# Kernel tuning notes

Hardware: AMD Instinct MI355X
Metric: run time of the kernel (lower is better)

Reference implementation:

```python
import jax, jax.numpy as jnp
import numpy as np

T, B, F = 512, 256, 1
H = 256          # hidden width of all GRU stacks
P = 256          # pred_classes
DELAY = 1
W_SCALE = 0.06   # ~1/sqrt(H), mimics torch GRUCell init scale


def setup_inputs() -> dict:
    key = jax.random.key(0)
    ks = jax.random.split(key, 24)
    rn = lambda k, shp, s=1.0: s * jax.random.normal(k, shp, dtype=jnp.float32)
    return {
        "sequence": rn(ks[0], (T, B, F)),
        "delay_pad": rn(ks[1], (DELAY, B, F)),
        "h0_enc": rn(ks[2], (B, H)),
        "h0_mask": rn(ks[3], (B, H)),
        "h0_pred": rn(ks[4], (B, H)),
        "enc_w_ih": rn(ks[5], (3 * H, F), W_SCALE),
        "enc_w_hh": rn(ks[6], (3 * H, H), W_SCALE),
        "enc_b_ih": rn(ks[7], (3 * H,), W_SCALE),
        "enc_b_hh": rn(ks[8], (3 * H,), W_SCALE),
        "mdec_w_ih": rn(ks[9], (3 * H, H), W_SCALE),
        "mdec_w_hh": rn(ks[10], (3 * H, H), W_SCALE),
        "mdec_b_ih": rn(ks[11], (3 * H,), W_SCALE),
        "mdec_b_hh": rn(ks[12], (3 * H,), W_SCALE),
        "mlin_w": rn(ks[13], (F, H), W_SCALE),
        "mlin_b": rn(ks[14], (F,), W_SCALE),
        "pdec_w_ih": rn(ks[15], (3 * H, H), W_SCALE),
        "pdec_w_hh": rn(ks[16], (3 * H, H), W_SCALE),
        "pdec_b_ih": rn(ks[17], (3 * H,), W_SCALE),
        "pdec_b_hh": rn(ks[18], (3 * H,), W_SCALE),
        "plin_w": rn(ks[19], (P, H), W_SCALE),
        "plin_b": rn(ks[20], (P,), W_SCALE),
    }


def gru_cell(x, h, w_ih, w_hh, b_ih, b_hh):
    # torch.nn.GRUCell semantics; gate order r, z, n in the stacked weights.
    gi = x @ w_ih.T + b_ih           # [B, 3H]
    gh = h @ w_hh.T + b_hh           # [B, 3H]
    i_r, i_z, i_n = jnp.split(gi, 3, axis=-1)
    h_r, h_z, h_n = jnp.split(gh, 3, axis=-1)
    r = jax.nn.sigmoid(i_r + h_r)
    z = jax.nn.sigmoid(i_z + h_z)
    n = jnp.tanh(i_n + r * h_n)
    return (1.0 - z) * n + z * h


def reference(sequence, delay_pad, h0_enc, h0_mask, h0_pred,
              enc_w_ih, enc_w_hh, enc_b_ih, enc_b_hh,
              mdec_w_ih, mdec_w_hh, mdec_b_ih, mdec_b_hh, mlin_w, mlin_b,
              pdec_w_ih, pdec_w_hh, pdec_b_ih, pdec_b_hh, plin_w, plin_b):
    # delay: prepend padding, drop last `delay` steps.  seq stays [T, B, F].
    seq = jnp.concatenate([delay_pad, sequence[:-DELAY]], axis=0)

    def step(carry, x_t):
        h_e, h_m, h_p = carry
        h_e = gru_cell(x_t, h_e, enc_w_ih, enc_w_hh, enc_b_ih, enc_b_hh)
        h_m = gru_cell(h_e, h_m, mdec_w_ih, mdec_w_hh, mdec_b_ih, mdec_b_hh)
        mask_t = h_m @ mlin_w.T + mlin_b      # [B, F]
        h_p = gru_cell(h_e, h_p, pdec_w_ih, pdec_w_hh, pdec_b_ih, pdec_b_hh)
        pred_t = h_p @ plin_w.T + plin_b      # [B, P]
        return (h_e, h_m, h_p), (mask_t, pred_t)

    _, (masks, preds) = jax.lax.scan(step, (h0_enc, h0_mask, h0_pred), seq)
    mask = masks.reshape(seq.shape)           # [T, B, F]
    pred = jnp.mean(preds, axis=0)            # [B, P]
    return mask, pred
```

## Files before the change

kernel.cpp:

```cpp
#include <hip/hip_runtime.h>
#include <hip/hip_fp16.h>

typedef _Float16 f16;
typedef _Float16 f16x8 __attribute__((ext_vector_type(8)));
typedef _Float16 f16x4 __attribute__((ext_vector_type(4)));
typedef float    f32x4 __attribute__((ext_vector_type(4)));

#define TT 512
#define BB 256
#define HH 256

#define O_WFRAG_ENC 0u
#define O_WFRAG_M   393216u
#define O_WFRAG_P   786432u
#define O_WFRAG_GI  1179648u
#define O_HE_ST     1966080u
#define O_HM_ST     2097152u
#define O_HP_ST     2228224u
#define O_HPSUM     2359296u
#define O_DYN       2621440u
#define DYN_PER_STEP 917504u

__device__ __forceinline__ float sigf(float x){ return 1.0f/(1.0f+__expf(-x)); }
__device__ __forceinline__ float tanh_(float x){
  float xc = fminf(fmaxf(x,-15.f),15.f);
  float e  = __expf(2.f*xc);
  return (e-1.f)/(e+1.f);
}
__device__ __forceinline__ int hswz(int row, int j){
  return row*256 + ((((j>>3) ^ (row&7)))<<3) + (j&7);
}
__device__ __forceinline__ void gload_lds16(const void* g, void* l){
  __builtin_amdgcn_global_load_lds(
      (const __attribute__((address_space(1))) unsigned int*)g,
      (__attribute__((address_space(3))) unsigned int*)l, 16, 0, 0);
}

__global__ void prep_kernel(
    const float* __restrict__ enc_whh, const float* __restrict__ mdec_whh,
    const float* __restrict__ pdec_whh, const float* __restrict__ mdec_wih,
    const float* __restrict__ pdec_wih,
    const float* __restrict__ h0e, const float* __restrict__ h0m, const float* __restrict__ h0p,
    f16* __restrict__ wfrag_enc, f16* __restrict__ wfrag_m, f16* __restrict__ wfrag_p,
    f16* __restrict__ wfrag_gi,
    f16* __restrict__ he_st, f16* __restrict__ hm_st, f16* __restrict__ hp_st,
    float* __restrict__ hpsum)
{
  int idx = blockIdx.x*256 + threadIdx.x;
  const int NW = 16*3*8*64*8;
  if (idx < 3*NW){
    int b = idx / NW, e = idx % NW;
    int jj = e & 7, l = (e>>3)&63, ks = (e>>9)&7, t2 = e>>12;
    int g = t2 % 3, w = t2 / 3;
    int row = g*256 + w*16 + (l&15);
    int col = ks*32 + (l>>4)*8 + jj;
    const float* W = (b==0)?enc_whh:((b==1)?mdec_whh:pdec_whh);
    f16* D = (b==0)?wfrag_enc:((b==1)?wfrag_m:wfrag_p);
    D[e] = (f16)W[row*256+col];
    return;
  }
  idx -= 3*NW;
  const int NG = 96*8*64*8;
  if (idx < NG){
    int e = idx;
    int jj = e&7, l=(e>>3)&63, ks=(e>>9)&7, mt = e>>12;
    int row = mt*16 + (l&15);
    int col = ks*32 + (l>>4)*8 + jj;
    float v = (row < 768) ? mdec_wih[row*256+col] : pdec_wih[(row-768)*256+col];
    wfrag_gi[e] = (f16)v;
    return;
  }
  idx -= NG;
  if (idx < 65536){
    he_st[idx] = (f16)h0e[idx];
    hm_st[idx] = (f16)h0m[idx];
    hp_st[idx] = (f16)h0p[idx];
    hpsum[idx] = 0.f;
  }
}

template<int MODE>
__device__ __forceinline__ void gru_run(
  int bt, int slice, int SL,
  const f16* __restrict__ wfrag,
  const float* __restrict__ bih, const float* __restrict__ bhh,
  const float* __restrict__ enc_wih,
  const float* __restrict__ seq, const float* __restrict__ dpad,
  const f16* __restrict__ gi_src,
  f16* __restrict__ h_state,
  f16* __restrict__ he_buf,
  const float* __restrict__ mlin_w, const float* __restrict__ mlin_b,
  float* __restrict__ out_mask,
  float* __restrict__ hpsum,
  unsigned char* smem)
{
  const int tid = threadIdx.x;
  const int lane = tid & 63;
  const int wid  = tid >> 6;
  const int l15  = lane & 15;
  const int lhi  = lane >> 4;
  const int bi0  = lhi*4;
  const int b0   = bt*16;

  f16* hbuf  = (f16*)smem;
  f16* gib   = (f16*)(smem + 16384);
  float* xb  = (float*)(smem + 16384 + 49152);
  float* mred = xb + 32;

  f16x8 wf[2][3][8];
  #pragma unroll
  for (int q=0;q<2;++q){
    const int w = wid*2+q;
    #pragma unroll
    for (int g=0;g<3;++g)
      #pragma unroll
      for (int ks=0;ks<8;++ks)
        wf[q][g][ks] = *(const f16x8*)(wfrag + ((size_t)(((w*3+g)*8)+ks)*64 + lane)*8);
  }
  #pragma unroll
  for (int q=0;q<2;++q)
    #pragma unroll
    for (int g=0;g<3;++g)
      #pragma unroll
      for (int ks=0;ks<8;++ks)
        asm volatile("" : "+v"(wf[q][g][ks]));

  float cr[2], cz[2], cnh[2], cni[2];
  float wr_[2], wz_[2], wn_[2], mw[2];
  #pragma unroll
  for (int q=0;q<2;++q){
    const int j = (wid*2+q)*16 + l15;
    cr[q]  = bih[j]     + bhh[j];
    cz[q]  = bih[256+j] + bhh[256+j];
    cnh[q] = bhh[512+j];
    cni[q] = bih[512+j];
    if (MODE==0){ wr_[q]=enc_wih[j]; wz_[q]=enc_wih[256+j]; wn_[q]=enc_wih[512+j]; }
    if (MODE==1){ mw[q]=mlin_w[j]; }
  }
  #pragma unroll
  for (int q=0;q<2;++q){
    const int j = (wid*2+q)*16 + l15;
    #pragma unroll
    for (int r=0;r<4;++r)
      hbuf[hswz(bi0+r, j)] = h_state[(size_t)(b0+bi0+r)*256 + j];
  }
  if (MODE==0){
    if (tid<16){
      const int t = slice*SL;
      xb[tid] = (t==0) ? dpad[b0+tid] : seq[(size_t)(t-1)*BB + b0 + tid];
    }
  } else {
    #pragma unroll
    for (int k=0;k<3;++k){
      const int c = wid*3 + k;
      gload_lds16((const char*)gi_src + c*1024 + (lane<<4),
                  (char*)gib + c*1024);
    }
  }
  __syncthreads();

  float psum[2][4];
  if (MODE==2){
    #pragma unroll
    for (int q=0;q<2;++q)
      #pragma unroll
      for (int r=0;r<4;++r) psum[q][r]=0.f;
  }

  for (int ts=0; ts<SL; ++ts){
    const int cur = ts & 1;
    f16* hc = hbuf + cur*4096;
    f16* hn = hbuf + (cur^1)*4096;

    if (MODE==0){
      if (tid<16 && ts+1<SL){
        const int t = slice*SL + ts + 1;
        xb[(cur^1)*16 + tid] = seq[(size_t)(t-1)*BB + b0 + tid];
      }
    } else {
      if (ts+1 < SL){
        const char* gsrc = (const char*)gi_src + (size_t)(ts+1)*786432u;
        char* gdst = (char*)gib + (cur^1)*24576;
        #pragma unroll
        for (int k=0;k<3;++k){
          const int c = wid*3 + k;
          gload_lds16(gsrc + c*1024 + (lane<<4), gdst + c*1024);
        }
      }
    }
    if (MODE==1){
      if (tid<16 && ts>0){
        float v = mlin_b[0];
        #pragma unroll
        for (int w=0;w<8;++w) v += mred[(cur^1)*128 + w*16 + tid];
        out_mask[(size_t)(slice*SL + ts-1)*BB + b0 + tid] = v;
      }
    }

    float mpart[4] = {0.f,0.f,0.f,0.f};
    #pragma unroll
    for (int q=0;q<2;++q){
      const int j = (wid*2+q)*16 + l15;
      f32x4 a0 = {cr[q],cr[q],cr[q],cr[q]};
      f32x4 a1 = {cz[q],cz[q],cz[q],cz[q]};
      f32x4 a2 = {cnh[q],cnh[q],cnh[q],cnh[q]};
      #pragma unroll
      for (int ks=0;ks<8;++ks){
        const f16x8 a = *(const f16x8*)(hc + l15*256 + ((((ks*4+lhi) ^ (l15&7)))<<3));
        a0 = __builtin_amdgcn_mfma_f32_16x16x32_f16(a, wf[q][0][ks], a0, 0,0,0);
        a1 = __builtin_amdgcn_mfma_f32_16x16x32_f16(a, wf[q][1][ks], a1, 0,0,0);
        a2 = __builtin_amdgcn_mfma_f32_16x16x32_f16(a, wf[q][2][ks], a2, 0,0,0);
      }
      float gir[4], giz[4], gin[4];
      if (MODE==0){
        #pragma unroll
        for (int r=0;r<4;++r){
          const float x = xb[cur*16 + bi0 + r];
          gir[r]=x*wr_[q]; giz[r]=x*wz_[q]; gin[r]=x*wn_[q];
        }
      } else {
        const f16* gb = gib + cur*12288;
        const f16x4 g0v = *(const f16x4*)(gb + j*16 + bi0);
        const f16x4 g1v = *(const f16x4*)(gb + (256+j)*16 + bi0);
        const f16x4 g2v = *(const f16x4*)(gb + (512+j)*16 + bi0);
        #pragma unroll
        for (int r=0;r<4;++r){ gir[r]=(float)g0v[r]; giz[r]=(float)g1v[r]; gin[r]=(float)g2v[r]; }
      }
      #pragma unroll
      for (int r=0;r<4;++r){
        const int sz = hswz(bi0+r, j);
        const float hprev = (float)hc[sz];
        const float rr = sigf(gir[r] + a0[r]);
        const float zz = sigf(giz[r] + a1[r]);
        const float nn = tanh_(gin[r] + cni[q] + rr*a2[r]);
        const float h  = (1.f-zz)*nn + zz*hprev;
        hn[sz] = (f16)h;
        if (MODE==0) he_buf[((size_t)ts*BB + (b0+bi0+r))*HH + j] = (f16)h;
        if (MODE==1) mpart[r] += h*mw[q];
        if (MODE==2) psum[q][r] += h;
      }
    }
    if (MODE==1){
      #pragma unroll
      for (int m=1;m<16;m<<=1){
        #pragma unroll
        for (int r=0;r<4;++r) mpart[r] += __shfl_xor(mpart[r], m, 64);
      }
      if (l15==0){
        #pragma unroll
        for (int r=0;r<4;++r) mred[cur*128 + wid*16 + bi0 + r] = mpart[r];
      }
    }
    __syncthreads();
  }

  if (MODE==1 && tid<16){
    float v = mlin_b[0];
    #pragma unroll
    for (int w=0;w<8;++w) v += mred[((SL-1)&1)*128 + w*16 + tid];
    out_mask[(size_t)(slice*SL + SL-1)*BB + b0 + tid] = v;
  }
  {
    const f16* hf = hbuf + (SL&1)*4096;
    #pragma unroll
    for (int q=0;q<2;++q){
      const int j = (wid*2+q)*16 + l15;
      #pragma unroll
      for (int r=0;r<4;++r)
        h_state[(size_t)(b0+bi0+r)*256 + j] = hf[hswz(bi0+r, j)];
    }
  }
  if (MODE==2){
    #pragma unroll
    for (int q=0;q<2;++q){
      const int j = (wid*2+q)*16 + l15;
      #pragma unroll
      for (int r=0;r<4;++r){
        const size_t idx = (size_t)(b0+bi0+r)*256 + j;
        hpsum[idx] = hpsum[idx] + psum[q][r];
      }
    }
  }
}

__global__ __launch_bounds__(512,1) void rec_kernel(
  const float* __restrict__ seq, const float* __restrict__ dpad,
  const float* __restrict__ enc_wih, const float* __restrict__ enc_bih, const float* __restrict__ enc_bhh,
  const float* __restrict__ mdec_bih, const float* __restrict__ mdec_bhh,
  const float* __restrict__ pdec_bih, const float* __restrict__ pdec_bhh,
  const float* __restrict__ mlin_w, const float* __restrict__ mlin_b,
  const f16* __restrict__ wfrag_enc, const f16* __restrict__ wfrag_m, const f16* __restrict__ wfrag_p,
  f16* __restrict__ he_st, f16* __restrict__ hm_st, f16* __restrict__ hp_st,
  f16* __restrict__ he_buf, const f16* __restrict__ gi_buf,
  float* __restrict__ hpsum, float* __restrict__ out_mask,
  int dec_slice, int enc_slice, int n_dec, int SL)
{
  __shared__ __align__(16) unsigned char smem[16384 + 49152 + 128 + 1024];
  const int bid = blockIdx.x;
  if (bid < n_dec){
    const int rec = bid >> 4, bt = bid & 15;
    const f16* gsrc = gi_buf + ((size_t)bt*1536 + (size_t)rec*768)*16;
    if (rec==0)
      gru_run<1>(bt, dec_slice, SL, wfrag_m, mdec_bih, mdec_bhh, nullptr, nullptr, nullptr,
                 gsrc, hm_st, nullptr, mlin_w, mlin_b, out_mask, nullptr, smem);
    else
      gru_run<2>(bt, dec_slice, SL, wfrag_p, pdec_bih, pdec_bhh, nullptr, nullptr, nullptr,
                 gsrc, hp_st, nullptr, nullptr, nullptr, nullptr, hpsum, smem);
  } else {
    const int bt = bid - n_dec;
    gru_run<0>(bt, enc_slice, SL, wfrag_enc, enc_bih, enc_bhh, enc_wih, seq, dpad,
               nullptr, he_st, he_buf, nullptr, nullptr, nullptr, nullptr, smem);
  }
}

__global__ __launch_bounds__(256,4) void gi_kernel(
  const f16* __restrict__ he_buf, const f16* __restrict__ wfrag_gi,
  f16* __restrict__ gi_buf)
{
  const int ts = blockIdx.x >> 2;
  const int bq = blockIdx.x & 3;
  const int tid = threadIdx.x, lane = tid&63, wid = tid>>6;
  const int l15 = lane&15, lhi = lane>>4;
  __shared__ f16 het[64*264];
  {
    const uint4* src = (const uint4*)(he_buf + ((size_t)ts*BB + bq*64)*HH);
    uint4* dst = (uint4*)het;
    #pragma unroll
    for (int k=0;k<8;++k){
      const int i = tid + k*256;
      dst[(i>>5)*33 + (i&31)] = src[i];
    }
  }
  __syncthreads();
  for (int mi=0; mi<24; ++mi){
    const int mt = wid*24 + mi;
    f32x4 acc[4] = {{0,0,0,0},{0,0,0,0},{0,0,0,0},{0,0,0,0}};
    #pragma unroll
    for (int ks=0;ks<8;++ks){
      const f16x8 a = *(const f16x8*)(wfrag_gi + ((size_t)(mt*8+ks)*64 + lane)*8);
      #pragma unroll
      for (int bt=0;bt<4;++bt){
        const f16x8 b = *(const f16x8*)(het + (bt*16+l15)*264 + ks*32 + lhi*8);
        acc[bt] = __builtin_amdgcn_mfma_f32_16x16x32_f16(a, b, acc[bt], 0,0,0);
      }
    }
    #pragma unroll
    for (int bt=0;bt<4;++bt){
      const int btg = bq*4 + bt;
      const size_t base = (((size_t)ts*16 + btg)*1536 + (size_t)mt*16 + lhi*4)*16 + l15;
      #pragma unroll
      for (int r=0;r<4;++r) gi_buf[base + (size_t)r*16] = (f16)acc[bt][r];
    }
  }
}

__global__ __launch_bounds__(256,1) void pred_kernel(
  const float* __restrict__ hpsum, const float* __restrict__ plin_w,
  const float* __restrict__ plin_b, float* __restrict__ out)
{
  __shared__ float hs[256];
  const int p = threadIdx.x;
  const float bias = plin_b[p];
  for (int bb=0; bb<4; ++bb){
    const int b = blockIdx.x*4 + bb;
    __syncthreads();
    hs[p] = hpsum[(size_t)b*256 + p];
    __syncthreads();
    float acc = 0.f;
    const float4* wrow = (const float4*)(plin_w + (size_t)p*256);
    #pragma unroll 4
    for (int k4=0;k4<64;++k4){
      const float4 w = wrow[k4];
      acc += hs[k4*4+0]*w.x + hs[k4*4+1]*w.y + hs[k4*4+2]*w.z + hs[k4*4+3]*w.w;
    }
    out[131072 + (size_t)b*256 + p] = acc*(1.f/512.f) + bias;
  }
}

extern "C" void kernel_launch(void* const* d_in, const int* in_sizes, int n_in,
                              void* d_out, int out_size, void* d_ws, size_t ws_size,
                              hipStream_t stream)
{
  const float* seq      = (const float*)d_in[0];
  const float* dpad     = (const float*)d_in[1];
  const float* h0e      = (const float*)d_in[2];
  const float* h0m      = (const float*)d_in[3];
  const float* h0p      = (const float*)d_in[4];
  const float* enc_wih  = (const float*)d_in[5];
  const float* enc_whh  = (const float*)d_in[6];
  const float* enc_bih  = (const float*)d_in[7];
  const float* enc_bhh  = (const float*)d_in[8];
  const float* mdec_wih = (const float*)d_in[9];
  const float* mdec_whh = (const float*)d_in[10];
  const float* mdec_bih = (const float*)d_in[11];
  const float* mdec_bhh = (const float*)d_in[12];
  const float* mlin_w   = (const float*)d_in[13];
  const float* mlin_b   = (const float*)d_in[14];
  const float* pdec_wih = (const float*)d_in[15];
  const float* pdec_whh = (const float*)d_in[16];
  const float* pdec_bih = (const float*)d_in[17];
  const float* pdec_bhh = (const float*)d_in[18];
  const float* plin_w   = (const float*)d_in[19];
  const float* plin_b   = (const float*)d_in[20];
  float* out = (float*)d_out;

  char* ws = (char*)d_ws;
  f16* wfrag_enc = (f16*)(ws + O_WFRAG_ENC);
  f16* wfrag_m   = (f16*)(ws + O_WFRAG_M);
  f16* wfrag_p   = (f16*)(ws + O_WFRAG_P);
  f16* wfrag_gi  = (f16*)(ws + O_WFRAG_GI);
  f16* he_st     = (f16*)(ws + O_HE_ST);
  f16* hm_st     = (f16*)(ws + O_HM_ST);
  f16* hp_st     = (f16*)(ws + O_HP_ST);
  float* hpsum   = (float*)(ws + O_HPSUM);

  int SL = 64;
  while (SL > 1 && (size_t)O_DYN + (size_t)SL*DYN_PER_STEP > ws_size) SL >>= 1;
  const int S = TT / SL;
  f16* he_buf = (f16*)(ws + O_DYN);
  f16* gi_buf = (f16*)(ws + O_DYN + (size_t)SL*131072u);

  prep_kernel<<<dim3(4096), dim3(256), 0, stream>>>(
      enc_whh, mdec_whh, pdec_whh, mdec_wih, pdec_wih, h0e, h0m, h0p,
      wfrag_enc, wfrag_m, wfrag_p, wfrag_gi, he_st, hm_st, hp_st, hpsum);

  rec_kernel<<<dim3(16), dim3(512), 0, stream>>>(
      seq, dpad, enc_wih, enc_bih, enc_bhh, mdec_bih, mdec_bhh, pdec_bih, pdec_bhh,
      mlin_w, mlin_b, wfrag_enc, wfrag_m, wfrag_p, he_st, hm_st, hp_st,
      he_buf, gi_buf, hpsum, out, 0, 0, 0, SL);
  gi_kernel<<<dim3(SL*4), dim3(256), 0, stream>>>(he_buf, wfrag_gi, gi_buf);

  for (int s=0; s<S; ++s){
    const int has_enc = (s+1 < S);
    rec_kernel<<<dim3(has_enc?48:32), dim3(512), 0, stream>>>(
        seq, dpad, enc_wih, enc_bih, enc_bhh, mdec_bih, mdec_bhh, pdec_bih, pdec_bhh,
        mlin_w, mlin_b, wfrag_enc, wfrag_m, wfrag_p, he_st, hm_st, hp_st,
        he_buf, gi_buf, hpsum, out, s, s+1, 32, SL);
    if (has_enc)
      gi_kernel<<<dim3(SL*4), dim3(256), 0, stream>>>(he_buf, wfrag_gi, gi_buf);
  }

  pred_kernel<<<dim3(64), dim3(256), 0, stream>>>(hpsum, plin_w, plin_b, out);
}
```

Before: 3.423 ms.

## Split each GRU recurrence across two cooperating blocks with flag-based hidden-state exchange

Each recurrent batch tile is now handled by a pair of 256-thread blocks, each owning half of the hidden units. After every timestep the two blocks exchange their halves of the new hidden state through global memory, using release/acquire flags and a spin-wait. This doubles the CUs working on the serial recurrence and halves the weight registers each block holds, at the cost of a per-step cross-block handshake. The change also folds the input biases into gi_kernel, reads gi values directly from global instead of staging them through LDS, and computes the mask projection with a separate in-block reduction; it relies on all 96 blocks being co-resident to avoid deadlock.

```diff
diff --git a/kernel.cpp b/kernel.cpp
--- a/kernel.cpp
+++ b/kernel.cpp
@@ -5,6 +5,8 @@
 typedef _Float16 f16x8 __attribute__((ext_vector_type(8)));
 typedef _Float16 f16x4 __attribute__((ext_vector_type(4)));
 typedef float    f32x4 __attribute__((ext_vector_type(4)));
+typedef unsigned long long u64;
+typedef u64 u64x2 __attribute__((ext_vector_type(2)));
 
 #define TT 512
 #define BB 256
@@ -18,7 +20,9 @@
 #define O_HM_ST     2097152u
 #define O_HP_ST     2228224u
 #define O_HPSUM     2359296u
-#define O_DYN       2621440u
+#define O_XCHG      2621440u
+#define O_FLAGS     3407872u
+#define O_DYN       3408896u
 #define DYN_PER_STEP 917504u
 
 __device__ __forceinline__ float sigf(float x){ return 1.0f/(1.0f+__expf(-x)); }
@@ -29,11 +33,6 @@
 }
 __device__ __forceinline__ int hswz(int row, int j){
   return row*256 + ((((j>>3) ^ (row&7)))<<3) + (j&7);
-}
-__device__ __forceinline__ void gload_lds16(const void* g, void* l){
-  __builtin_amdgcn_global_load_lds(
-      (const __attribute__((address_space(1))) unsigned int*)g,
-      (__attribute__((address_space(3))) unsigned int*)l, 16, 0, 0);
 }
 
 __global__ void prep_kernel(
@@ -44,7 +43,7 @@
     f16* __restrict__ wfrag_enc, f16* __restrict__ wfrag_m, f16* __restrict__ wfrag_p,
     f16* __restrict__ wfrag_gi,
     f16* __restrict__ he_st, f16* __restrict__ hm_st, f16* __restrict__ hp_st,
-    float* __restrict__ hpsum)
+    float* __restrict__ hpsum, int* __restrict__ flags)
 {
   int idx = blockIdx.x*256 + threadIdx.x;
   const int NW = 16*3*8*64*8;
@@ -76,12 +75,13 @@
     hm_st[idx] = (f16)h0m[idx];
     hp_st[idx] = (f16)h0p[idx];
     hpsum[idx] = 0.f;
+    if (idx < 96) flags[idx] = 0;
   }
 }
 
 template<int MODE>
 __device__ __forceinline__ void gru_run(
-  int bt, int slice, int SL,
+  int role, int bt, int slice, int SL,
   const f16* __restrict__ wfrag,
   const float* __restrict__ bih, const float* __restrict__ bhh,
   const float* __restrict__ enc_wih,
@@ -92,6 +92,7 @@
   const float* __restrict__ mlin_w, const float* __restrict__ mlin_b,
   float* __restrict__ out_mask,
   float* __restrict__ hpsum,
+  u64* __restrict__ xchg, int* __restrict__ flags,
   unsigned char* smem)
 {
   const int tid = threadIdx.x;
@@ -101,16 +102,16 @@
   const int lhi  = lane >> 4;
   const int bi0  = lhi*4;
   const int b0   = bt*16;
-
-  f16* hbuf  = (f16*)smem;
-  f16* gib   = (f16*)(smem + 16384);
-  float* xb  = (float*)(smem + 16384 + 49152);
-  float* mred = xb + 32;
+  constexpr int FREC = (MODE==1) ? 0 : ((MODE==2) ? 1 : 2);
+
+  f16* hbuf   = (f16*)smem;
+  float* xb   = (float*)(smem + 16384);
+  float* mlwf = xb + 32;
 
   f16x8 wf[2][3][8];
   #pragma unroll
   for (int q=0;q<2;++q){
-    const int w = wid*2+q;
+    const int w = role*8 + wid*2 + q;
     #pragma unroll
     for (int g=0;g<3;++g)
       #pragma unroll
@@ -126,20 +127,30 @@
         asm volatile("" : "+v"(wf[q][g][ks]));
 
   float cr[2], cz[2], cnh[2], cni[2];
-  float wr_[2], wz_[2], wn_[2], mw[2];
+  float wr_[2], wz_[2], wn_[2];
   #pragma unroll
   for (int q=0;q<2;++q){
-    const int j = (wid*2+q)*16 + l15;
-    cr[q]  = bih[j]     + bhh[j];
-    cz[q]  = bih[256+j] + bhh[256+j];
-    cnh[q] = bhh[512+j];
-    cni[q] = bih[512+j];
-    if (MODE==0){ wr_[q]=enc_wih[j]; wz_[q]=enc_wih[256+j]; wn_[q]=enc_wih[512+j]; }
-    if (MODE==1){ mw[q]=mlin_w[j]; }
-  }
-  #pragma unroll
-  for (int q=0;q<2;++q){
-    const int j = (wid*2+q)*16 + l15;
+    const int j = (role*8 + wid*2 + q)*16 + l15;
+    if (MODE==0){
+      cr[q]  = bih[j]     + bhh[j];
+      cz[q]  = bih[256+j] + bhh[256+j];
+      cnh[q] = bhh[512+j];
+      cni[q] = bih[512+j];
+      wr_[q]=enc_wih[j]; wz_[q]=enc_wih[256+j]; wn_[q]=enc_wih[512+j];
+    } else {
+      cr[q]  = bhh[j];
+      cz[q]  = bhh[256+j];
+      cnh[q] = bhh[512+j];
+    }
+  }
+  float mlb = 0.f;
+  if (MODE==1 && role==0){
+    mlwf[tid] = mlin_w[tid];
+    mlb = mlin_b[0];
+  }
+
+  for (int jb=wid; jb<16; jb+=4){
+    const int j = jb*16 + l15;
     #pragma unroll
     for (int r=0;r<4;++r)
       hbuf[hswz(bi0+r, j)] = h_state[(size_t)(b0+bi0+r)*256 + j];
@@ -149,13 +160,6 @@
       const int t = slice*SL;
       xb[tid] = (t==0) ? dpad[b0+tid] : seq[(size_t)(t-1)*BB + b0 + tid];
     }
-  } else {
-    #pragma unroll
-    for (int k=0;k<3;++k){
-      const int c = wid*3 + k;
-      gload_lds16((const char*)gi_src + c*1024 + (lane<<4),
-                  (char*)gib + c*1024);
-    }
   }
   __syncthreads();
 
@@ -166,41 +170,44 @@
       #pragma unroll
       for (int r=0;r<4;++r) psum[q][r]=0.f;
   }
+
+  const int fmy = (FREC*16 + bt)*2 + role;
+  const int fpt = (FREC*16 + bt)*2 + (1-role);
+  int* myf = flags + fmy;
+  int* ptf = flags + fpt;
 
   for (int ts=0; ts<SL; ++ts){
     const int cur = ts & 1;
     f16* hc = hbuf + cur*4096;
     f16* hn = hbuf + (cur^1)*4096;
-
-    if (MODE==0){
-      if (tid<16 && ts+1<SL){
-        const int t = slice*SL + ts + 1;
-        xb[(cur^1)*16 + tid] = seq[(size_t)(t-1)*BB + b0 + tid];
-      }
+    const int gstep = slice*SL + ts;
+
+    f16x4 gv[2][3];
+    if (MODE!=0){
+      const f16* gts = gi_src + (size_t)ts*393216u;
+      #pragma unroll
+      for (int q=0;q<2;++q)
+        #pragma unroll
+        for (int g=0;g<3;++g)
+          gv[q][g] = *(const f16x4*)(gts + ((size_t)(g*256 + (role*8+wid*2+q)*16 + l15))*16 + bi0);
     } else {
-      if (ts+1 < SL){
-        const char* gsrc = (const char*)gi_src + (size_t)(ts+1)*786432u;
-        char* gdst = (char*)gib + (cur^1)*24576;
-        #pragma unroll
-        for (int k=0;k<3;++k){
-          const int c = wid*3 + k;
-          gload_lds16(gsrc + c*1024 + (lane<<4), gdst + c*1024);
-        }
-      }
-    }
-    if (MODE==1){
-      if (tid<16 && ts>0){
-        float v = mlin_b[0];
-        #pragma unroll
-        for (int w=0;w<8;++w) v += mred[(cur^1)*128 + w*16 + tid];
-        out_mask[(size_t)(slice*SL + ts-1)*BB + b0 + tid] = v;
-      }
-    }
-
-    float mpart[4] = {0.f,0.f,0.f,0.f};
+      if (tid<16 && ts+1<SL)
+        xb[(cur^1)*16 + tid] = seq[(size_t)(slice*SL + ts)*BB + b0 + tid];
+    }
+
+    if (MODE==1 && role==0 && ts>0){
+      const int mb = tid>>4, jj = tid&15;
+      float s = 0.f;
+      #pragma unroll
+      for (int k=0;k<16;++k){ const int j = jj + k*16; s += (float)hc[hswz(mb, j)]*mlwf[j]; }
+      s += __shfl_xor(s,1,64); s += __shfl_xor(s,2,64);
+      s += __shfl_xor(s,4,64); s += __shfl_xor(s,8,64);
+      if (jj==0) out_mask[(size_t)(slice*SL + ts-1)*BB + b0 + mb] = s + mlb;
+    }
+
     #pragma unroll
     for (int q=0;q<2;++q){
-      const int j = (wid*2+q)*16 + l15;
+      const int j = (role*8 + wid*2 + q)*16 + l15;
       f32x4 a0 = {cr[q],cr[q],cr[q],cr[q]};
       f32x4 a1 = {cz[q],cz[q],cz[q],cz[q]};
       f32x4 a2 = {cnh[q],cnh[q],cnh[q],cnh[q]};
@@ -216,15 +223,13 @@
         #pragma unroll
         for (int r=0;r<4;++r){
           const float x = xb[cur*16 + bi0 + r];
-          gir[r]=x*wr_[q]; giz[r]=x*wz_[q]; gin[r]=x*wn_[q];
+          gir[r]=x*wr_[q]; giz[r]=x*wz_[q]; gin[r]=x*wn_[q] + cni[q];
         }
       } else {
-        const f16* gb = gib + cur*12288;
-        const f16x4 g0v = *(const f16x4*)(gb + j*16 + bi0);
-        const f16x4 g1v = *(const f16x4*)(gb + (256+j)*16 + bi0);
-        const f16x4 g2v = *(const f16x4*)(gb + (512+j)*16 + bi0);
         #pragma unroll
-        for (int r=0;r<4;++r){ gir[r]=(float)g0v[r]; giz[r]=(float)g1v[r]; gin[r]=(float)g2v[r]; }
+        for (int r=0;r<4;++r){
+          gir[r]=(float)gv[q][0][r]; giz[r]=(float)gv[q][1][r]; gin[r]=(float)gv[q][2][r];
+        }
       }
       #pragma unroll
       for (int r=0;r<4;++r){
@@ -232,48 +237,65 @@
         const float hprev = (float)hc[sz];
         const float rr = sigf(gir[r] + a0[r]);
         const float zz = sigf(giz[r] + a1[r]);
-        const float nn = tanh_(gin[r] + cni[q] + rr*a2[r]);
+        const float nn = tanh_(gin[r] + rr*a2[r]);
         const float h  = (1.f-zz)*nn + zz*hprev;
         hn[sz] = (f16)h;
         if (MODE==0) he_buf[((size_t)ts*BB + (b0+bi0+r))*HH + j] = (f16)h;
-        if (MODE==1) mpart[r] += h*mw[q];
         if (MODE==2) psum[q][r] += h;
       }
     }
-    if (MODE==1){
-      #pragma unroll
-      for (int m=1;m<16;m<<=1){
-        #pragma unroll
-        for (int r=0;r<4;++r) mpart[r] += __shfl_xor(mpart[r], m, 64);
-      }
-      if (l15==0){
-        #pragma unroll
-        for (int r=0;r<4;++r) mred[cur*128 + wid*16 + bi0 + r] = mpart[r];
-      }
-    }
-    __syncthreads();
-  }
-
-  if (MODE==1 && tid<16){
-    float v = mlin_b[0];
-    #pragma unroll
-    for (int w=0;w<8;++w) v += mred[((SL-1)&1)*128 + w*16 + tid];
-    out_mask[(size_t)(slice*SL + SL-1)*BB + b0 + tid] = v;
-  }
-  {
-    const f16* hf = hbuf + (SL&1)*4096;
+    __syncthreads();
+
+    {
+      const int trow = tid>>4, tgl = tid&15;
+      const int glo = tgl + role*16;
+      const f16* sp = hn + trow*256 + ((glo ^ (trow&7))<<3);
+      const u64x2 v = *(const u64x2*)sp;
+      u64* dm = xchg + ((size_t)(fmy*2 + cur))*512 + tid*2;
+      __hip_atomic_store(dm+0, v[0], __ATOMIC_RELAXED, __HIP_MEMORY_SCOPE_AGENT);
+      __hip_atomic_store(dm+1, v[1], __ATOMIC_RELAXED, __HIP_MEMORY_SCOPE_AGENT);
+    }
+    __syncthreads();
+    if (tid==0){
+      __hip_atomic_store(myf, gstep+1, __ATOMIC_RELEASE, __HIP_MEMORY_SCOPE_AGENT);
+      while (__hip_atomic_load(ptf, __ATOMIC_ACQUIRE, __HIP_MEMORY_SCOPE_AGENT) < gstep+1)
+        __builtin_amdgcn_s_sleep(1);
+    }
+    __syncthreads();
+    {
+      const int trow = tid>>4, tgl = tid&15;
+      const u64* dp = xchg + ((size_t)(fpt*2 + cur))*512 + tid*2;
+      u64x2 v;
+      v[0] = __hip_atomic_load(dp+0, __ATOMIC_RELAXED, __HIP_MEMORY_SCOPE_AGENT);
+      v[1] = __hip_atomic_load(dp+1, __ATOMIC_RELAXED, __HIP_MEMORY_SCOPE_AGENT);
+      const int glp = tgl + (1-role)*16;
+      f16* dq = hn + trow*256 + ((glp ^ (trow&7))<<3);
+      *(u64x2*)dq = v;
+    }
+    __syncthreads();
+  }
+
+  const f16* hf = hbuf + (SL&1)*4096;
+  if (MODE==1 && role==0){
+    const int mb = tid>>4, jj = tid&15;
+    float s = 0.f;
+    #pragma unroll
+    for (int k=0;k<16;++k){ const int j = jj + k*16; s += (float)hf[hswz(mb, j)]*mlwf[j]; }
+    s += __shfl_xor(s,1,64); s += __shfl_xor(s,2,64);
+    s += __shfl_xor(s,4,64); s += __shfl_xor(s,8,64);
+    if (jj==0) out_mask[(size_t)(slice*SL + SL-1)*BB + b0 + mb] = s + mlb;
+  }
+  #pragma unroll
+  for (int q=0;q<2;++q){
+    const int j = (role*8 + wid*2 + q)*16 + l15;
+    #pragma unroll
+    for (int r=0;r<4;++r)
+      h_state[(size_t)(b0+bi0+r)*256 + j] = hf[hswz(bi0+r, j)];
+  }
+  if (MODE==2){
     #pragma unroll
     for (int q=0;q<2;++q){
-      const int j = (wid*2+q)*16 + l15;
-      #pragma unroll
-      for (int r=0;r<4;++r)
-        h_state[(size_t)(b0+bi0+r)*256 + j] = hf[hswz(bi0+r, j)];
-    }
-  }
-  if (MODE==2){
-    #pragma unroll
-    for (int q=0;q<2;++q){
-      const int j = (wid*2+q)*16 + l15;
+      const int j = (role*8 + wid*2 + q)*16 + l15;
       #pragma unroll
       for (int r=0;r<4;++r){
         const size_t idx = (size_t)(b0+bi0+r)*256 + j;
@@ -283,38 +305,45 @@
   }
 }
 
-__global__ __launch_bounds__(512,1) void rec_kernel(
+__global__ __launch_bounds__(256,1) void rec_kernel(
   const float* __restrict__ seq, const float* __restrict__ dpad,
   const float* __restrict__ enc_wih, const float* __restrict__ enc_bih, const float* __restrict__ enc_bhh,
-  const float* __restrict__ mdec_bih, const float* __restrict__ mdec_bhh,
-  const float* __restrict__ pdec_bih, const float* __restrict__ pdec_bhh,
+  const float* __restrict__ mdec_bhh, const float* __restrict__ pdec_bhh,
   const float* __restrict__ mlin_w, const float* __restrict__ mlin_b,
   const f16* __restrict__ wfrag_enc, const f16* __restrict__ wfrag_m, const f16* __restrict__ wfrag_p,
   f16* __restrict__ he_st, f16* __restrict__ hm_st, f16* __restrict__ hp_st,
   f16* __restrict__ he_buf, const f16* __restrict__ gi_buf,
   float* __restrict__ hpsum, float* __restrict__ out_mask,
-  int dec_slice, int enc_slice, int n_dec, int SL)
-{
-  __shared__ __align__(16) unsigned char smem[16384 + 49152 + 128 + 1024];
+  u64* __restrict__ xchg, int* __restrict__ flags,
+  int dec_slice, int enc_slice, int SL)
+{
+  __shared__ __align__(16) unsigned char smem[16384 + 128 + 1024 + 512];
   const int bid = blockIdx.x;
-  if (bid < n_dec){
-    const int rec = bid >> 4, bt = bid & 15;
-    const f16* gsrc = gi_buf + ((size_t)bt*1536 + (size_t)rec*768)*16;
-    if (rec==0)
-      gru_run<1>(bt, dec_slice, SL, wfrag_m, mdec_bih, mdec_bhh, nullptr, nullptr, nullptr,
-                 gsrc, hm_st, nullptr, mlin_w, mlin_b, out_mask, nullptr, smem);
-    else
-      gru_run<2>(bt, dec_slice, SL, wfrag_p, pdec_bih, pdec_bhh, nullptr, nullptr, nullptr,
-                 gsrc, hp_st, nullptr, nullptr, nullptr, nullptr, hpsum, smem);
+  const int pp = bid % 48, role = bid / 48;
+  if (pp < 16){
+    if (dec_slice < 0) return;
+    const int bt = pp;
+    gru_run<1>(role, bt, dec_slice, SL, wfrag_m, nullptr, mdec_bhh, nullptr, nullptr, nullptr,
+               gi_buf + (size_t)bt*1536*16, hm_st, nullptr, mlin_w, mlin_b, out_mask, nullptr,
+               xchg, flags, smem);
+  } else if (pp < 32){
+    if (dec_slice < 0) return;
+    const int bt = pp - 16;
+    gru_run<2>(role, bt, dec_slice, SL, wfrag_p, nullptr, pdec_bhh, nullptr, nullptr, nullptr,
+               gi_buf + ((size_t)bt*1536 + 768)*16, hp_st, nullptr, nullptr, nullptr, nullptr, hpsum,
+               xchg, flags, smem);
   } else {
-    const int bt = bid - n_dec;
-    gru_run<0>(bt, enc_slice, SL, wfrag_enc, enc_bih, enc_bhh, enc_wih, seq, dpad,
-               nullptr, he_st, he_buf, nullptr, nullptr, nullptr, nullptr, smem);
+    if (enc_slice < 0) return;
+    const int bt = pp - 32;
+    gru_run<0>(role, bt, enc_slice, SL, wfrag_enc, enc_bih, enc_bhh, enc_wih, seq, dpad,
+               nullptr, he_st, he_buf, nullptr, nullptr, nullptr, nullptr,
+               xchg, flags, smem);
   }
 }
 
 __global__ __launch_bounds__(256,4) void gi_kernel(
   const f16* __restrict__ he_buf, const f16* __restrict__ wfrag_gi,
+  const float* __restrict__ mdec_bih, const float* __restrict__ pdec_bih,
   f16* __restrict__ gi_buf)
 {
   const int ts = blockIdx.x >> 2;
@@ -334,6 +363,13 @@
   __syncthreads();
   for (int mi=0; mi<24; ++mi){
     const int mt = wid*24 + mi;
+    const int row0 = mt*16 + lhi*4;
+    float bb[4];
+    #pragma unroll
+    for (int r=0;r<4;++r){
+      const int rw = row0 + r;
+      bb[r] = (rw < 768) ? mdec_bih[rw] : pdec_bih[rw-768];
+    }
     f32x4 acc[4] = {{0,0,0,0},{0,0,0,0},{0,0,0,0},{0,0,0,0}};
     #pragma unroll
     for (int ks=0;ks<8;++ks){
@@ -349,7 +385,7 @@
       const int btg = bq*4 + bt;
       const size_t base = (((size_t)ts*16 + btg)*1536 + (size_t)mt*16 + lhi*4)*16 + l15;
       #pragma unroll
-      for (int r=0;r<4;++r) gi_buf[base + (size_t)r*16] = (f16)acc[bt][r];
+      for (int r=0;r<4;++r) gi_buf[base + (size_t)r*16] = (f16)(acc[bt][r] + bb[r]);
     }
   }
 }
@@ -413,6 +449,8 @@
   f16* hm_st     = (f16*)(ws + O_HM_ST);
   f16* hp_st     = (f16*)(ws + O_HP_ST);
   float* hpsum   = (float*)(ws + O_HPSUM);
+  u64* xchg      = (u64*)(ws + O_XCHG);
+  int* flags     = (int*)(ws + O_FLAGS);
 
   int SL = 64;
   while (SL > 1 && (size_t)O_DYN + (size_t)SL*DYN_PER_STEP > ws_size) SL >>= 1;
@@ -422,22 +460,22 @@
 
   prep_kernel<<<dim3(4096), dim3(256), 0, stream>>>(
       enc_whh, mdec_whh, pdec_whh, mdec_wih, pdec_wih, h0e, h0m, h0p,
-      wfrag_enc, wfrag_m, wfrag_p, wfrag_gi, he_st, hm_st, hp_st, hpsum);
-
-  rec_kernel<<<dim3(16), dim3(512), 0, stream>>>(
-      seq, dpad, enc_wih, enc_bih, enc_bhh, mdec_bih, mdec_bhh, pdec_bih, pdec_bhh,
+      wfrag_enc, wfrag_m, wfrag_p, wfrag_gi, he_st, hm_st, hp_st, hpsum, flags);
+
+  rec_kernel<<<dim3(96), dim3(256), 0, stream>>>(
+      seq, dpad, enc_wih, enc_bih, enc_bhh, mdec_bhh, pdec_bhh,
       mlin_w, mlin_b, wfrag_enc, wfrag_m, wfrag_p, he_st, hm_st, hp_st,
-      he_buf, gi_buf, hpsum, out, 0, 0, 0, SL);
-  gi_kernel<<<dim3(SL*4), dim3(256), 0, stream>>>(he_buf, wfrag_gi, gi_buf);
+      he_buf, gi_buf, hpsum, out, xchg, flags, -1, 0, SL);
+  gi_kernel<<<dim3(SL*4), dim3(256), 0, stream>>>(he_buf, wfrag_gi, mdec_bih, pdec_bih, gi_buf);
 
   for (int s=0; s<S; ++s){
-    const int has_enc = (s+1 < S);
-    rec_kernel<<<dim3(has_enc?48:32), dim3(512), 0, stream>>>(
-        seq, dpad, enc_wih, enc_bih, enc_bhh, mdec_bih, mdec_bhh, pdec_bih, pdec_bhh,
+    const int enc_s = (s+1 < S) ? (s+1) : -1;
+    rec_kernel<<<dim3(96), dim3(256), 0, stream>>>(
+        seq, dpad, enc_wih, enc_bih, enc_bhh, mdec_bhh, pdec_bhh,
         mlin_w, mlin_b, wfrag_enc, wfrag_m, wfrag_p, he_st, hm_st, hp_st,
-        he_buf, gi_buf, hpsum, out, s, s+1, 32, SL);
-    if (has_enc)
-      gi_kernel<<<dim3(SL*4), dim3(256), 0, stream>>>(he_buf, wfrag_gi, gi_buf);
+        he_buf, gi_buf, hpsum, out, xchg, flags, s, enc_s, SL);
+    if (enc_s >= 0)
+      gi_kernel<<<dim3(SL*4), dim3(256), 0, stream>>>(he_buf, wfrag_gi, mdec_bih, pdec_bih, gi_buf);
   }
 
   pred_kernel<<<dim3(64), dim3(256), 0, stream>>>(hpsum, plin_w, plin_b, out);
```

After: 3.918 ms. 14.5% more time.
